# Kernel optimization log

Measured on AMD Instinct MI355X. Metric: run time of the kernel, lower is better.

The kernel has to match this reference:

```python
import jax, jax.numpy as jnp
import numpy as np
from jax import lax

T, S = 2000, 100          # trees, nodes per tree
N = T * S                 # total nodes
F = 256                   # in_feats (sent_hidden_size)
H = 256                   # h_feats (prop_hidden_size)


def _build_forest():
    # Random recursive forest: node j in each tree attaches to a uniform earlier node.
    rng = np.random.default_rng(0)
    pl = np.zeros((T, S), np.int64)    # local parent index
    dep = np.zeros((T, S), np.int64)
    rows = np.arange(T)
    for j in range(1, S):
        p = rng.integers(0, j, size=T)
        pl[:, j] = p
        dep[:, j] = dep[rows, p] + 1
    depth = dep.ravel()
    parent = (np.arange(T)[:, None] * S + pl).ravel()
    is_root = (np.arange(N) % S) == 0
    kids = np.arange(N)[~is_root]
    par = parent[~is_root]
    order = np.argsort(par, kind='stable')
    kids_s, par_s = kids[order], par[order]
    counts = np.bincount(par_s, minlength=N)
    C = int(counts.max())
    offsets = np.concatenate([[0], np.cumsum(counts)])
    pos = np.arange(len(kids_s)) - offsets[par_s]
    ch_all = np.full((N, C), N + 1, np.int32)   # pad with dummy zero-hidden row N+1
    ch_all[par_s, pos] = kids_s
    maxd = int(depth.max())
    L = maxd  # processed layers: depths 0..maxd-1 (deepest leaves stay zero, as in torch)
    layer_lists = [np.where(depth == d)[0] for d in range(L)]
    M = max(len(l) for l in layer_lists)
    layer_nodes = np.full((L, M), N, np.int32)  # pad writes to scratch row N
    child_idx = np.full((L, M, C), N + 1, np.int32)
    child_cnt = np.zeros((L, M), np.int32)
    for d, nd in enumerate(layer_lists):
        m = len(nd)
        layer_nodes[d, :m] = nd
        child_idx[d, :m] = ch_all[nd]
        child_cnt[d, :m] = counts[nd]
    root_idx = (np.arange(T) * S).astype(np.int32)
    return layer_nodes, child_idx, child_cnt, root_idx


def setup_inputs() -> dict:
    layer_nodes, child_idx, child_cnt, root_idx = _build_forest()
    key = jax.random.key(0)
    k1, k2, k3, k4, k5 = jax.random.split(key, 5)
    bound = 1.0 / np.sqrt(H)  # torch GRUCell default init
    u = lambda kk, sh: jax.random.uniform(kk, sh, jnp.float32, -bound, bound)
    return {
        'inputs': jax.random.normal(k1, (N, F), jnp.float32),
        'w_ih': u(k2, (3 * H, F)),
        'w_hh': u(k3, (3 * H, H)),
        'b_ih': u(k4, (3 * H,)),
        'b_hh': u(k5, (3 * H,)),
        'layer_nodes': jnp.asarray(layer_nodes),
        'child_idx': jnp.asarray(child_idx),
        'child_cnt': jnp.asarray(child_cnt),
        'root_idx': jnp.asarray(root_idx),
    }


def _gru(x, h, w_ih, w_hh, b_ih, b_hh):
    gi = x @ w_ih.T + b_ih
    gh = h @ w_hh.T + b_hh
    ir, iz, ig = jnp.split(gi, 3, axis=-1)
    hr, hz, hg = jnp.split(gh, 3, axis=-1)
    r = jax.nn.sigmoid(ir + hr)
    z = jax.nn.sigmoid(iz + hz)
    n = jnp.tanh(ig + r * hg)
    return (1.0 - z) * n + z * h


def _forward(inputs, w_ih, w_hh, b_ih, b_hh, layer_nodes, child_idx, child_cnt, root_idx):
    # rows N (scatter scratch for padded slots) and N+1 (always-zero child pad) appended
    x_all = jnp.concatenate([inputs, jnp.zeros((2, F), inputs.dtype)], axis=0)
    h0 = jnp.zeros((N + 2, H), inputs.dtype)

    def step(all_h, layer):
        nodes, cidx, ccnt = layer
        ch = all_h[cidx]                                        # [M, C, H]
        denom = jnp.maximum(ccnt, 1).astype(all_h.dtype)[:, None]
        h_prev = ch.sum(axis=1) / denom                         # mean over children; 0 for leaves
        new_h = _gru(x_all[nodes], h_prev, w_ih, w_hh, b_ih, b_hh)
        return all_h.at[nodes].set(new_h), None

    # process deepest layer first (reversed(range(max_depth)) in the original)
    xs = (layer_nodes[::-1], child_idx[::-1], child_cnt[::-1])
    all_h, _ = lax.scan(step, h0, xs)
    return all_h[root_idx]                                      # [T, H]


def reference(inputs, w_ih, w_hh, b_ih, b_hh, layer_nodes, child_idx, child_cnt, root_idx):
    return _forward(inputs, w_ih, w_hh, b_ih, b_hh, layer_nodes, child_idx, child_cnt, root_idx)
```

## Files before the change

### kernel.cpp

```cpp
#include <hip/hip_runtime.h>
#include <hip/hip_bf16.h>
#include <math.h>

#define N_NODES 200000
#define T_TREES 2000
#define S_NODES 100
#define F_DIM 256
#define H_DIM 256
#define G_DIM 768
#define D_MAX 24

typedef __attribute__((ext_vector_type(8))) short short8b;
typedef __attribute__((ext_vector_type(4))) float f32x4;

static __device__ __forceinline__ unsigned short f2bf(float x) {
    union { __hip_bfloat16 h; unsigned short u; } cv;
    cv.h = __float2bfloat16(x);
    return cv.u;
}
static __device__ __forceinline__ float bf2f(unsigned short u) {
    return __uint_as_float(((unsigned)u) << 16);
}
static __device__ __forceinline__ float fsig(float x) {
    return __builtin_amdgcn_rcpf(1.0f + __expf(-x));
}
static __device__ __forceinline__ float ftanh(float x) {
    return 1.0f - 2.0f * __builtin_amdgcn_rcpf(__expf(2.0f * x) + 1.0f);
}

__global__ void k_zero(float4* __restrict__ p, int n4) {
    float4 z = make_float4(0.f, 0.f, 0.f, 0.f);
    for (int i = blockIdx.x * blockDim.x + threadIdx.x; i < n4;
         i += gridDim.x * blockDim.x)
        p[i] = z;
}

__global__ void k_convx(const float* __restrict__ x, unsigned short* __restrict__ xb,
                        int n8) {
    for (int i = blockIdx.x * blockDim.x + threadIdx.x; i < n8;
         i += gridDim.x * blockDim.x) {
        const float4* px = (const float4*)(x + (size_t)i * 8);
        float4 u = px[0], v = px[1];
        short8b t;
        t[0] = f2bf(u.x); t[1] = f2bf(u.y); t[2] = f2bf(u.z); t[3] = f2bf(u.w);
        t[4] = f2bf(v.x); t[5] = f2bf(v.y); t[6] = f2bf(v.z); t[7] = f2bf(v.w);
        *(short8b*)(xb + (size_t)i * 8) = t;
    }
}

__global__ void k_findM(const int* __restrict__ ln, int LM, int* __restrict__ Mdev) {
    int local = 0x7F7F7F7F;
    for (int p = T_TREES + blockIdx.x * blockDim.x + threadIdx.x; p < LM;
         p += gridDim.x * blockDim.x)
        if (ln[p] < N_NODES && p < local) local = p;
#pragma unroll
    for (int off = 32; off; off >>= 1) {
        int o = __shfl_down(local, off);
        if (o < local) local = o;
    }
    __shared__ int wmin[4];
    if ((threadIdx.x & 63) == 0) wmin[threadIdx.x >> 6] = local;
    __syncthreads();
    if (threadIdx.x == 0) {
        int m = wmin[0];
        for (int i = 1; i < 4; ++i) if (wmin[i] < m) m = wmin[i];
        if (m < 0x7F7F7F7F) atomicMin(Mdev, m);
    }
}

__global__ void k_hist(const int* __restrict__ ln, const int* __restrict__ Mdev,
                       int* __restrict__ layer_cnt, int LM) {
    __shared__ int h[D_MAX];
    if (threadIdx.x < D_MAX) h[threadIdx.x] = 0;
    __syncthreads();
    const int M = Mdev[0];
    for (int p = blockIdx.x * blockDim.x + threadIdx.x; p < LM;
         p += gridDim.x * blockDim.x)
        if (ln[p] < N_NODES) {
            int d = p / M;
            if (d < D_MAX) atomicAdd(&h[d], 1);
        }
    __syncthreads();
    if (threadIdx.x < D_MAX && h[threadIdx.x])
        atomicAdd(&layer_cnt[threadIdx.x], h[threadIdx.x]);
}

__global__ void k_convw(const float* __restrict__ wi, const float* __restrict__ wh,
                        unsigned short* __restrict__ wib, unsigned short* __restrict__ whb) {
    int i = blockIdx.x * blockDim.x + threadIdx.x;
    if (i < G_DIM * F_DIM) {
        wib[i] = f2bf(wi[i]);
        whb[i] = f2bf(wh[i]);
    }
}

__global__ __launch_bounds__(256) void k_gemm_x(
    const unsigned short* __restrict__ xb,
    const unsigned short* __restrict__ wib,
    const float* __restrict__ b_ih,
    unsigned short* __restrict__ gi_all) {
    __shared__ unsigned short Bs[2][64][256];

    const int tid = threadIdx.x;
    const int wv = tid >> 6, lane = tid & 63;
    const int lr = lane & 15, kg = lane >> 4;
    const long m0 = (long)blockIdx.x * 128 + wv * 32;

    short8b A[2][8];
#pragma unroll
    for (int ms = 0; ms < 2; ++ms) {
        long r = m0 + ms * 16 + lr;
        if (r > N_NODES - 1) r = N_NODES - 1;
        const unsigned short* xp = xb + r * F_DIM + kg * 8;
#pragma unroll
        for (int ks = 0; ks < 8; ++ks)
            A[ms][ks] = *(const short8b*)(xp + ks * 32);
    }

    const int sr = tid >> 2, sp = tid & 3;
    const int hs = (sr & 3) | (((sr >> 3) & 1) << 2);
    const int gp_off = (lr >> 2) * 8 + (lr & 3);
    const int hq = (lr & 3) | (((lr >> 2) & 1) << 2);

    short8b st[8];
    {
        const unsigned short* src = wib + (size_t)sr * F_DIM;
#pragma unroll
        for (int q = 0; q < 4; ++q) {
            int c = sp * 16 + q * 64;
            st[2 * q]     = *(const short8b*)(src + c);
            st[2 * q + 1] = *(const short8b*)(src + c + 8);
        }
#pragma unroll
        for (int q = 0; q < 4; ++q) {
            int c0 = sp * 2 + q * 8, c1 = c0 + 1;
            *(short8b*)&Bs[0][sr][((c0 & 24) | ((c0 ^ hs) & 7)) << 3] = st[2 * q];
            *(short8b*)&Bs[0][sr][((c1 & 24) | ((c1 ^ hs) & 7)) << 3] = st[2 * q + 1];
        }
    }
    __syncthreads();

    const f32x4 zf = {0.f, 0.f, 0.f, 0.f};

    for (int nt = 0; nt < 12; ++nt) {
        const int cur = nt & 1;
        if (nt < 11) {
            const unsigned short* src = wib + (size_t)((nt + 1) * 64 + sr) * F_DIM;
#pragma unroll
            for (int q = 0; q < 4; ++q) {
                int c = sp * 16 + q * 64;
                st[2 * q]     = *(const short8b*)(src + c);
                st[2 * q + 1] = *(const short8b*)(src + c + 8);
            }
        }
#pragma unroll
        for (int nsp = 0; nsp < 2; ++nsp) {
            f32x4 aP0 = zf, aQ0 = zf, aP1 = zf, aQ1 = zf;
            const int rP = nsp * 32 + gp_off;
#pragma unroll
            for (int ks = 0; ks < 8; ++ks) {
                const int c = ks * 4 + kg;
                const int pc = ((c & 24) | ((c ^ hq) & 7)) << 3;
                short8b BP = *(const short8b*)&Bs[cur][rP][pc];
                short8b BQ = *(const short8b*)&Bs[cur][rP + 4][pc];
                aP0 = __builtin_amdgcn_mfma_f32_16x16x32_bf16(BP, A[0][ks], aP0, 0, 0, 0);
                aQ0 = __builtin_amdgcn_mfma_f32_16x16x32_bf16(BQ, A[0][ks], aQ0, 0, 0, 0);
                aP1 = __builtin_amdgcn_mfma_f32_16x16x32_bf16(BP, A[1][ks], aP1, 0, 0, 0);
                aQ1 = __builtin_amdgcn_mfma_f32_16x16x32_bf16(BQ, A[1][ks], aQ1, 0, 0, 0);
            }
            const int g0 = nt * 64 + nsp * 32 + kg * 8;
            f32x4 b0 = *(const f32x4*)(b_ih + g0);
            f32x4 b1 = *(const f32x4*)(b_ih + g0 + 4);
            long m = m0 + lr;
            if (m < N_NODES) {
                short8b pk;
#pragma unroll
                for (int i = 0; i < 4; ++i) {
                    pk[i]     = f2bf(aP0[i] + b0[i]);
                    pk[4 + i] = f2bf(aQ0[i] + b1[i]);
                }
                *(short8b*)(gi_all + m * G_DIM + g0) = pk;
            }
            m = m0 + 16 + lr;
            if (m < N_NODES) {
                short8b pk;
#pragma unroll
                for (int i = 0; i < 4; ++i) {
                    pk[i]     = f2bf(aP1[i] + b0[i]);
                    pk[4 + i] = f2bf(aQ1[i] + b1[i]);
                }
                *(short8b*)(gi_all + m * G_DIM + g0) = pk;
            }
        }
        if (nt < 11) {
            __syncthreads();
#pragma unroll
            for (int q = 0; q < 4; ++q) {
                int c0 = sp * 2 + q * 8, c1 = c0 + 1;
                *(short8b*)&Bs[cur ^ 1][sr][((c0 & 24) | ((c0 ^ hs) & 7)) << 3] = st[2 * q];
                *(short8b*)&Bs[cur ^ 1][sr][((c1 & 24) | ((c1 ^ hs) & 7)) << 3] = st[2 * q + 1];
            }
            __syncthreads();
        }
    }
}

#define LOADC2(buf, ns_, kh_)                                                  \
  _Pragma("unroll")                                                            \
  for (int kk = 0; kk < 4; ++kk)                                               \
    buf[kk] = *(const short8b*)(whb +                                          \
        (size_t)(512 + cb + (ns_) * 16 + lr) * H_DIM + ((kh_) * 4 + kk) * 32 + kg * 8);

#define MMACP(c_)                                                              \
  _Pragma("unroll")                                                            \
  for (int ks = 0; ks < 8; ++ks) {                                             \
    const int cch = ks * 4 + kg;                                               \
    const int pc = ((cch & 24) | ((cch ^ lr) & 7)) << 3;                       \
    short8b A0 = *(const short8b*)&Ab[lr][pc];                                 \
    short8b A1 = *(const short8b*)&Ab[16 + lr][pc];                            \
    _Pragma("unroll")                                                          \
    for (int ns = 0; ns < 2; ++ns) {                                           \
      acc[c_][0][ns] = __builtin_amdgcn_mfma_f32_16x16x32_bf16(                \
          A0, Bp[c_][ns][ks], acc[c_][0][ns], 0, 0, 0);                        \
      acc[c_][1][ns] = __builtin_amdgcn_mfma_f32_16x16x32_bf16(                \
          A1, Bp[c_][ns][ks], acc[c_][1][ns], 0, 0, 0);                        \
    }                                                                          \
  }

#define MMAC2(buf, ns_, kh_)                                                   \
  _Pragma("unroll")                                                            \
  for (int kk = 0; kk < 4; ++kk) {                                             \
    const int ks = (kh_) * 4 + kk;                                             \
    const int cch = ks * 4 + kg;                                               \
    const int pc = ((cch & 24) | ((cch ^ lr) & 7)) << 3;                       \
    short8b A0 = *(const short8b*)&Ab[lr][pc];                                 \
    short8b A1 = *(const short8b*)&Ab[16 + lr][pc];                            \
    acc[2][0][ns_] = __builtin_amdgcn_mfma_f32_16x16x32_bf16(                  \
        A0, buf[kk], acc[2][0][ns_], 0, 0, 0);                                 \
    acc[2][1][ns_] = __builtin_amdgcn_mfma_f32_16x16x32_bf16(                  \
        A1, buf[kk], acc[2][1][ns_], 0, 0, 0);                                 \
  }

__global__ __launch_bounds__(512, 2) void k_layer(
    const int* __restrict__ layer_nodes,
    const int* __restrict__ child_idx,
    const int* __restrict__ child_cnt,
    const int* __restrict__ Mdev,
    const int* __restrict__ layer_cnt,
    const unsigned short* __restrict__ whb,
    const unsigned short* __restrict__ gi_all,
    const float* __restrict__ b_hh,
    unsigned short* __restrict__ h_all,
    float* __restrict__ out,
    int d, int C) {
    __shared__ unsigned short Ab[32][256];
    __shared__ unsigned short Ag[32][776];
    __shared__ int Nd[32];

    const int cntd = layer_cnt[d];
    if (cntd == 0) return;
    const int M = Mdev[0];
    const int ntiles = (cntd + 31) >> 5;
    if (blockIdx.x >= ntiles) return;
    const long pbase = (long)d * M;

    const int tid = threadIdx.x;
    const int wv = tid >> 6, lane = tid & 63;
    const int lr = lane & 15, kg = lane >> 4;
    const int cb = wv * 32;

    short8b Bp[2][2][8];
#pragma unroll
    for (int c = 0; c < 2; ++c)
#pragma unroll
        for (int ns = 0; ns < 2; ++ns) {
            const unsigned short* bp =
                whb + (size_t)(c * 256 + cb + ns * 16 + lr) * H_DIM + kg * 8;
#pragma unroll
            for (int ks = 0; ks < 8; ++ks)
                Bp[c][ns][ks] = *(const short8b*)(bp + ks * 32);
        }

    float bh[3][2];
#pragma unroll
    for (int c = 0; c < 3; ++c)
#pragma unroll
        for (int ns = 0; ns < 2; ++ns)
            bh[c][ns] = b_hh[c * 256 + cb + ns * 16 + lr];

    const int srow = tid >> 4;
    const int sc = tid & 15;

    for (int tile = blockIdx.x; tile < ntiles; tile += gridDim.x) {
        __syncthreads();
        {
            int idx = tile * 32 + srow;
            int node = (idx < cntd) ? layer_nodes[pbase + idx] : -1;
            if (sc == 0) Nd[srow] = node;
            {
                const unsigned short* gp =
                    gi_all + (size_t)(node >= 0 ? node : 0) * G_DIM;
#pragma unroll
                for (int pass = 0; pass < 6; ++pass) {
                    int col = sc * 8 + pass * 128;
                    *(short8b*)&Ag[srow][col] = *(const short8b*)(gp + col);
                }
            }
            int cc = 0;
            const int* ch = nullptr;
            if (node >= 0) {
                cc = child_cnt[pbase + idx];
                ch = child_idx + (size_t)(pbase + idx) * C;
            }
            float inv = 1.0f / (float)(cc > 0 ? cc : 1);
            float sum[16];
#pragma unroll
            for (int i = 0; i < 16; ++i) sum[i] = 0.f;
#pragma unroll 2
            for (int c = 0; c < cc; ++c) {
                int kid = ch[c];
                const unsigned short* hr = h_all + (size_t)kid * H_DIM + sc * 16;
                short8b v0 = *(const short8b*)hr;
                short8b v1 = *(const short8b*)(hr + 8);
#pragma unroll
                for (int i = 0; i < 8; ++i) {
                    sum[i]     += bf2f((unsigned short)v0[i]);
                    sum[8 + i] += bf2f((unsigned short)v1[i]);
                }
            }
            short8b q0, q1;
#pragma unroll
            for (int i = 0; i < 8; ++i) {
                q0[i] = f2bf(sum[i] * inv);
                q1[i] = f2bf(sum[8 + i] * inv);
            }
            const int g = srow & 7;
            const int c0 = 2 * sc, c1 = 2 * sc + 1;
            *(short8b*)&Ab[srow][((c0 & 24) | ((c0 ^ g) & 7)) << 3] = q0;
            *(short8b*)&Ab[srow][((c1 & 24) | ((c1 ^ g) & 7)) << 3] = q1;
        }
        __syncthreads();

        const f32x4 zf = {0.f, 0.f, 0.f, 0.f};
        f32x4 acc[3][2][2];
#pragma unroll
        for (int c = 0; c < 3; ++c)
#pragma unroll
            for (int ms = 0; ms < 2; ++ms)
#pragma unroll
                for (int ns = 0; ns < 2; ++ns) acc[c][ms][ns] = zf;

        short8b C2a[4], C2b[4];
        LOADC2(C2a, 0, 0);
        MMACP(0);
        LOADC2(C2b, 0, 1);
        MMAC2(C2a, 0, 0);
        LOADC2(C2a, 1, 0);
        MMACP(1);
        MMAC2(C2b, 0, 1);
        LOADC2(C2b, 1, 1);
        MMAC2(C2a, 1, 0);
        MMAC2(C2b, 1, 1);

#pragma unroll
        for (int ms = 0; ms < 2; ++ms)
#pragma unroll
            for (int i = 0; i < 4; ++i) {
                const int rl = ms * 16 + kg * 4 + i;
                const int nd = Nd[rl];
                if (nd < 0) continue;
#pragma unroll
                for (int ns = 0; ns < 2; ++ns) {
                    const int k = cb + ns * 16 + lr;
                    const int kc = k >> 3;
                    const int hp_off = (((kc & 24) | ((kc ^ rl) & 7)) << 3) + (k & 7);
                    float hp = bf2f(Ab[rl][hp_off]);
                    float xr = bf2f(Ag[rl][k])       + acc[0][ms][ns][i] + bh[0][ns];
                    float xz = bf2f(Ag[rl][256 + k]) + acc[1][ms][ns][i] + bh[1][ns];
                    float r = fsig(xr);
                    float z = fsig(xz);
                    float n = ftanh(bf2f(Ag[rl][512 + k]) +
                                    r * (acc[2][ms][ns][i] + bh[2][ns]));
                    float h = (1.0f - z) * n + z * hp;
                    if (d == 0) {
                        out[(size_t)(nd / S_NODES) * H_DIM + k] = h;
                    } else {
                        h_all[(size_t)nd * H_DIM + k] = f2bf(h);
                    }
                }
            }
    }
}

extern "C" void kernel_launch(void* const* d_in, const int* in_sizes, int n_in,
                              void* d_out, int out_size, void* d_ws, size_t ws_size,
                              hipStream_t stream) {
    const float* inputs = (const float*)d_in[0];
    const float* w_ih   = (const float*)d_in[1];
    const float* w_hh   = (const float*)d_in[2];
    const float* b_ih   = (const float*)d_in[3];
    const float* b_hh   = (const float*)d_in[4];
    const int* layer_nodes = (const int*)d_in[5];
    const int* child_idx   = (const int*)d_in[6];
    const int* child_cnt   = (const int*)d_in[7];

    const int LM = in_sizes[5];
    const int C  = in_sizes[6] / in_sizes[5];

    char* w = (char*)d_ws;
    size_t o = 0;
    auto alloc = [&](size_t bytes) {
        void* p = w + o;
        o += (bytes + 255) & ~(size_t)255;
        return p;
    };
    unsigned short* wib    = (unsigned short*)alloc((size_t)G_DIM * F_DIM * 2);
    unsigned short* whb    = (unsigned short*)alloc((size_t)G_DIM * H_DIM * 2);
    unsigned short* xb     = (unsigned short*)alloc((size_t)N_NODES * F_DIM * 2);
    unsigned short* h_all  = (unsigned short*)alloc((size_t)N_NODES * H_DIM * 2);
    unsigned short* gi_all = (unsigned short*)alloc((size_t)N_NODES * G_DIM * 2);
    int*            Mdev      = (int*)alloc(4);
    int*            layer_cnt = (int*)alloc(D_MAX * 4);
    (void)ws_size;

    hipMemsetAsync(Mdev, 0x7F, 4, stream);
    hipMemsetAsync(layer_cnt, 0, D_MAX * 4, stream);

    k_zero<<<2048, 256, 0, stream>>>((float4*)h_all, N_NODES * H_DIM * 2 / 16);
    k_convx<<<2048, 256, 0, stream>>>(inputs, xb, N_NODES * F_DIM / 8);
    k_findM<<<256, 256, 0, stream>>>(layer_nodes, LM, Mdev);
    k_hist<<<256, 256, 0, stream>>>(layer_nodes, Mdev, layer_cnt, LM);
    k_convw<<<(G_DIM * F_DIM + 255) / 256, 256, 0, stream>>>(w_ih, w_hh, wib, whb);

    k_gemm_x<<<(N_NODES + 127) / 128, 256, 0, stream>>>(xb, wib, b_ih, gi_all);

    for (int d = D_MAX - 1; d >= 0; --d)
        k_layer<<<512, 512, 0, stream>>>(layer_nodes, child_idx, child_cnt,
                                         Mdev, layer_cnt, whb, gi_all, b_hh,
                                         h_all, (float*)d_out, d, C);
}
```

Before: 1.017 ms.

## Handle leaf nodes in a separate elementwise kernel, compact internal nodes per layer

Leaf nodes (no children) have zero previous hidden state, so their GRU output depends only on the input gates and biases. A new elementwise kernel computes all leaves except roots up front, skipping the W_hh matmul for them. A compaction kernel builds per-depth lists of internal nodes (plus roots), so the per-layer MFMA kernel only tiles over nodes that need the recurrent matmul. This adds an atomic compaction pass and an indirection, and the order of nodes within each layer is no longer deterministic.

```diff
diff --git a/kernel.cpp b/kernel.cpp
--- a/kernel.cpp
+++ b/kernel.cpp
@@ -68,21 +68,23 @@
     }
 }
 
-__global__ void k_hist(const int* __restrict__ ln, const int* __restrict__ Mdev,
-                       int* __restrict__ layer_cnt, int LM) {
-    __shared__ int h[D_MAX];
-    if (threadIdx.x < D_MAX) h[threadIdx.x] = 0;
-    __syncthreads();
+__global__ void k_compact(const int* __restrict__ ln,
+                          const int* __restrict__ child_cnt,
+                          const int* __restrict__ Mdev,
+                          int* __restrict__ int_cnt,
+                          int* __restrict__ int_pos,
+                          int LM) {
     const int M = Mdev[0];
     for (int p = blockIdx.x * blockDim.x + threadIdx.x; p < LM;
-         p += gridDim.x * blockDim.x)
-        if (ln[p] < N_NODES) {
+         p += gridDim.x * blockDim.x) {
+        if (ln[p] < N_NODES && (child_cnt[p] > 0 || p < M)) {
             int d = p / M;
-            if (d < D_MAX) atomicAdd(&h[d], 1);
-        }
-    __syncthreads();
-    if (threadIdx.x < D_MAX && h[threadIdx.x])
-        atomicAdd(&layer_cnt[threadIdx.x], h[threadIdx.x]);
+            if (d < D_MAX) {
+                int slot = atomicAdd(&int_cnt[d], 1);
+                int_pos[(size_t)d * M + slot] = p;
+            }
+        }
+    }
 }
 
 __global__ void k_convw(const float* __restrict__ wi, const float* __restrict__ wh,
@@ -201,6 +203,52 @@
                 *(short8b*)&Bs[cur ^ 1][sr][((c1 & 24) | ((c1 ^ hs) & 7)) << 3] = st[2 * q + 1];
             }
             __syncthreads();
+        }
+    }
+}
+
+__global__ void k_leaf(const int* __restrict__ ln,
+                       const int* __restrict__ child_cnt,
+                       const int* __restrict__ Mdev,
+                       const unsigned short* __restrict__ gi_all,
+                       const float* __restrict__ b_hh,
+                       unsigned short* __restrict__ h_all,
+                       int LM) {
+    const int M = Mdev[0];
+    const int total = LM * 8;
+    for (int t = blockIdx.x * blockDim.x + threadIdx.x; t < total;
+         t += gridDim.x * blockDim.x) {
+        const int p = t >> 3;
+        if (p < M) continue;
+        const int node = ln[p];
+        if (node >= N_NODES || child_cnt[p] != 0) continue;
+        const int cb = (t & 7) * 32;
+        const unsigned short* gp = gi_all + (size_t)node * G_DIM;
+        unsigned short* hw = h_all + (size_t)node * H_DIM;
+#pragma unroll
+        for (int q = 0; q < 4; ++q) {
+            const int k = cb + q * 8;
+            short8b gr = *(const short8b*)(gp + k);
+            short8b gz = *(const short8b*)(gp + 256 + k);
+            short8b gn = *(const short8b*)(gp + 512 + k);
+            f32x4 br0 = *(const f32x4*)(b_hh + k);
+            f32x4 br1 = *(const f32x4*)(b_hh + k + 4);
+            f32x4 bz0 = *(const f32x4*)(b_hh + 256 + k);
+            f32x4 bz1 = *(const f32x4*)(b_hh + 256 + k + 4);
+            f32x4 bn0 = *(const f32x4*)(b_hh + 512 + k);
+            f32x4 bn1 = *(const f32x4*)(b_hh + 512 + k + 4);
+            short8b ph;
+#pragma unroll
+            for (int j = 0; j < 8; ++j) {
+                float bhr = (j < 4) ? br0[j] : br1[j - 4];
+                float bhz = (j < 4) ? bz0[j] : bz1[j - 4];
+                float bhn = (j < 4) ? bn0[j] : bn1[j - 4];
+                float r = fsig(bf2f((unsigned short)gr[j]) + bhr);
+                float z = fsig(bf2f((unsigned short)gz[j]) + bhz);
+                float n = ftanh(bf2f((unsigned short)gn[j]) + r * bhn);
+                ph[j] = f2bf((1.0f - z) * n);
+            }
+            *(short8b*)(hw + k) = ph;
         }
     }
 }
@@ -246,7 +294,8 @@
     const int* __restrict__ child_idx,
     const int* __restrict__ child_cnt,
     const int* __restrict__ Mdev,
-    const int* __restrict__ layer_cnt,
+    const int* __restrict__ int_cnt,
+    const int* __restrict__ int_pos,
     const unsigned short* __restrict__ whb,
     const unsigned short* __restrict__ gi_all,
     const float* __restrict__ b_hh,
@@ -257,10 +306,10 @@
     __shared__ unsigned short Ag[32][776];
     __shared__ int Nd[32];
 
-    const int cntd = layer_cnt[d];
-    if (cntd == 0) return;
+    const int icnt = int_cnt[d];
+    if (icnt == 0) return;
     const int M = Mdev[0];
-    const int ntiles = (cntd + 31) >> 5;
+    const int ntiles = (icnt + 31) >> 5;
     if (blockIdx.x >= ntiles) return;
     const long pbase = (long)d * M;
 
@@ -294,8 +343,9 @@
     for (int tile = blockIdx.x; tile < ntiles; tile += gridDim.x) {
         __syncthreads();
         {
-            int idx = tile * 32 + srow;
-            int node = (idx < cntd) ? layer_nodes[pbase + idx] : -1;
+            int slot = tile * 32 + srow;
+            int p = (slot < icnt) ? int_pos[pbase + slot] : -1;
+            int node = (p >= 0) ? layer_nodes[p] : -1;
             if (sc == 0) Nd[srow] = node;
             {
                 const unsigned short* gp =
@@ -308,9 +358,9 @@
             }
             int cc = 0;
             const int* ch = nullptr;
-            if (node >= 0) {
-                cc = child_cnt[pbase + idx];
-                ch = child_idx + (size_t)(pbase + idx) * C;
+            if (p >= 0) {
+                cc = child_cnt[p];
+                ch = child_idx + (size_t)p * C;
             }
             float inv = 1.0f / (float)(cc > 0 ? cc : 1);
             float sum[16];
@@ -419,23 +469,28 @@
     unsigned short* xb     = (unsigned short*)alloc((size_t)N_NODES * F_DIM * 2);
     unsigned short* h_all  = (unsigned short*)alloc((size_t)N_NODES * H_DIM * 2);
     unsigned short* gi_all = (unsigned short*)alloc((size_t)N_NODES * G_DIM * 2);
+    int*            int_pos   = (int*)alloc((size_t)LM * 4);
     int*            Mdev      = (int*)alloc(4);
-    int*            layer_cnt = (int*)alloc(D_MAX * 4);
+    int*            int_cnt   = (int*)alloc(D_MAX * 4);
     (void)ws_size;
 
     hipMemsetAsync(Mdev, 0x7F, 4, stream);
-    hipMemsetAsync(layer_cnt, 0, D_MAX * 4, stream);
+    hipMemsetAsync(int_cnt, 0, D_MAX * 4, stream);
 
     k_zero<<<2048, 256, 0, stream>>>((float4*)h_all, N_NODES * H_DIM * 2 / 16);
     k_convx<<<2048, 256, 0, stream>>>(inputs, xb, N_NODES * F_DIM / 8);
     k_findM<<<256, 256, 0, stream>>>(layer_nodes, LM, Mdev);
-    k_hist<<<256, 256, 0, stream>>>(layer_nodes, Mdev, layer_cnt, LM);
+    k_compact<<<512, 256, 0, stream>>>(layer_nodes, child_cnt, Mdev,
+                                       int_cnt, int_pos, LM);
     k_convw<<<(G_DIM * F_DIM + 255) / 256, 256, 0, stream>>>(w_ih, w_hh, wib, whb);
 
     k_gemm_x<<<(N_NODES + 127) / 128, 256, 0, stream>>>(xb, wib, b_ih, gi_all);
+
+    k_leaf<<<2048, 256, 0, stream>>>(layer_nodes, child_cnt, Mdev,
+                                     gi_all, b_hh, h_all, LM);
 
     for (int d = D_MAX - 1; d >= 0; --d)
         k_layer<<<512, 512, 0, stream>>>(layer_nodes, child_idx, child_cnt,
-                                         Mdev, layer_cnt, whb, gi_all, b_hh,
-                                         h_all, (float*)d_out, d, C);
-}
+                                         Mdev, int_cnt, int_pos, whb, gi_all,
+                                         b_hh, h_all, (float*)d_out, d, C);
+}
```

Measured after the change: 2.131 ms. 2.1x slower.
